# Kernel tuning notes

Measured on AMD Instinct MI355X. Metric: run time of the kernel, lower is better.

The kernel has to match this reference:

```python
import jax, jax.numpy as jnp
import numpy as np

B, N, D = 4, 4096, 512      # batch, seq_len, model width
DIM_K = 64                   # per-head key dim used ONLY for the 1/sqrt scale
PROJ = 512                   # dim_k*heads = dim_v*heads = 64*8


def setup_inputs() -> dict:
    key = jax.random.key(0)
    ks = jax.random.split(key, 11)
    glorot = lambda k, shape: jax.random.uniform(
        k, shape, jnp.float32,
        -np.sqrt(6.0 / (shape[0] + shape[1])), np.sqrt(6.0 / (shape[0] + shape[1])))
    return {
        "q": jax.random.normal(ks[0], (B, N, D), jnp.float32),
        "k": jax.random.normal(ks[1], (B, N, D), jnp.float32),
        "v": jax.random.normal(ks[2], (B, N, D), jnp.float32),
        "w_q": glorot(ks[3], (D, PROJ)),
        "w_k": glorot(ks[4], (D, PROJ)),
        "w_v": glorot(ks[5], (D, PROJ)),
        "w_mha": glorot(ks[6], (PROJ, D)),
        "b_q": jnp.zeros((1, 1, PROJ), jnp.float32),
        "b_k": jnp.zeros((1, 1, PROJ), jnp.float32),
        "b_v": jnp.zeros((1, 1, PROJ), jnp.float32),
        "b_mha": jnp.zeros((1, 1, D), jnp.float32),
    }


def reference(q, k, v, w_q, w_k, w_v, w_mha, b_q, b_k, b_v, b_mha):
    # Projections (tensordot over last axis + broadcast bias)
    qp = jnp.einsum('bnd,de->bne', q, w_q) + b_q
    kp = jnp.einsum('bnd,de->bne', k, w_k) + b_k
    vp = jnp.einsum('bnd,de->bne', v, w_v) + b_v
    # NOTE: original call() forgets to pass heads=self.heads, so heads=1:
    # a single attention over the full PROJ width, scaled by sqrt(DIM_K).
    atts = jnp.einsum('bqe,bke->bqk', qp, kp) / np.sqrt(DIM_K).astype(np.float32)
    atts = jax.nn.softmax(atts, axis=-1)      # [B, N, N]
    dpa = jnp.einsum('bqk,bke->bqe', atts, vp)
    return jnp.einsum('bne,ed->bnd', dpa, w_mha) + b_mha
```

## Files before the change

kernel.cpp:

```cpp
#include <hip/hip_runtime.h>
#include <hip/hip_bf16.h>


typedef __attribute__((ext_vector_type(8))) short bf16x8;
typedef __attribute__((ext_vector_type(4))) float f32x4;

#define NB 4
#define NN 4096
#define ND 512

__device__ __forceinline__ f32x4 mfma16(bf16x8 a, bf16x8 b, f32x4 c) {
    return __builtin_amdgcn_mfma_f32_16x16x32_bf16(a, b, c, 0, 0, 0);
}
__device__ __forceinline__ short f2bf(float f) {
    __hip_bfloat16 h = __float2bfloat16(f);
    return *reinterpret_cast<short*>(&h);
}

typedef __attribute__((address_space(1))) const unsigned int gls_gt;
typedef __attribute__((address_space(3))) unsigned int gls_lt;
__device__ __forceinline__ void gll16(const void* g, void* l) {
    __builtin_amdgcn_global_load_lds((gls_gt*)g, (gls_lt*)l, 16, 0, 0);
}

#define DPP_ROR_STEP(V, CTRL, OP)                                              \
    {                                                                          \
        int _t = __builtin_amdgcn_update_dpp(0, __float_as_int(V), (CTRL),     \
                                             0xf, 0xf, true);                  \
        (V) = OP((V), __int_as_float(_t));                                     \
    }
__device__ __forceinline__ float faddf(float a, float b) { return a + b; }
__device__ __forceinline__ float rmax16(float v) {
    DPP_ROR_STEP(v, 0x128, fmaxf)
    DPP_ROR_STEP(v, 0x124, fmaxf)
    DPP_ROR_STEP(v, 0x122, fmaxf)
    DPP_ROR_STEP(v, 0x121, fmaxf)
    return v;
}
__device__ __forceinline__ float rsum16(float v) {
    DPP_ROR_STEP(v, 0x128, faddf)
    DPP_ROR_STEP(v, 0x124, faddf)
    DPP_ROR_STEP(v, 0x122, faddf)
    DPP_ROR_STEP(v, 0x121, faddf)
    return v;
}

struct Ptrs4 {
    const float* in[4];
    short* out[4];
};

__global__ void transpose_w(Ptrs4 p) {
    __shared__ short tile[32][33];
    const float* in = p.in[blockIdx.z];
    short* out = p.out[blockIdx.z];
    int r0 = blockIdx.y * 32, c0 = blockIdx.x * 32;
    int tx = threadIdx.x, ty = threadIdx.y;
    for (int i = 0; i < 32; i += 8)
        tile[ty + i][tx] = f2bf(in[(r0 + ty + i) * 512 + c0 + tx]);
    __syncthreads();
    for (int i = 0; i < 32; i += 8)
        out[(c0 + ty + i) * 512 + r0 + tx] = tile[tx][ty + i];
}

struct ProjArgs {
    const float* in[3];
    const short* wt[3];
    const float* bias[3];
    short* out[3];
};

__global__ __launch_bounds__(256, 2) void proj_gemm3(ProjArgs pp) {
    __shared__ __align__(1024) char As[2][16384];
    __shared__ __align__(1024) char Bs[2][16384];
    int z = blockIdx.z;
    const float* A32 = pp.in[z];
    const short* Bt = pp.wt[z];
    const float* bias = pp.bias[z];
    short* C = pp.out[z];

    int tid = threadIdx.x;
    int lane = tid & 63, w = tid >> 6;
    int l15 = lane & 15, l4 = lane >> 4;
    int wr2 = (w & 1) * 64, wc2 = (w >> 1) * 64;
    int m0 = blockIdx.x * 128, n0 = blockIdx.y * 128;
    f32x4 acc[16] = {};

    int sr = lane >> 3;
    int sd = ((lane & 7) ^ sr) << 3;

#define P_STAGE_B(BUF, KT)                                                  \
    {                                                                       \
        _Pragma("unroll")                                                   \
        for (int i = 0; i < 4; i++) {                                       \
            int rbase = i * 32 + w * 8;                                     \
            gll16(&Bt[(size_t)(n0 + rbase + sr) * 512 + (KT) + sd],         \
                  Bs[BUF] + rbase * 128);                                   \
        }                                                                   \
    }

    float4 areg[8];
    int arow = w * 32 + (lane >> 4);
    int akc = lane & 15;
#define P_LOAD_A32(KT)                                                      \
    {                                                                       \
        _Pragma("unroll")                                                   \
        for (int inst = 0; inst < 8; inst++)                                \
            areg[inst] = ((const float4*)(A32 +                             \
                (size_t)(m0 + arow + inst * 4) * 512 + (KT)))[akc];         \
    }
#define P_WRITE_A32(BUF)                                                    \
    {                                                                       \
        _Pragma("unroll")                                                   \
        for (int inst = 0; inst < 8; inst++) {                              \
            int r = arow + inst * 4;                                        \
            short pk[4];                                                    \
            pk[0] = f2bf(areg[inst].x); pk[1] = f2bf(areg[inst].y);         \
            pk[2] = f2bf(areg[inst].z); pk[3] = f2bf(areg[inst].w);         \
            *(long long*)(As[BUF] + r * 128 +                               \
                (((akc >> 1) ^ (r & 7)) << 4) + ((akc & 1) << 3)) =         \
                *(const long long*)pk;                                      \
        }                                                                   \
    }

    P_LOAD_A32(0);
    P_STAGE_B(0, 0);
    P_WRITE_A32(0);
    for (int t = 0; t < 8; t++) {
        __syncthreads();
        if (t < 7) {
            P_LOAD_A32((t + 1) * 64);
            P_STAGE_B((t + 1) & 1, (t + 1) * 64);
        }
        const char* Ab = As[t & 1];
        const char* Bb = Bs[t & 1];
#pragma unroll
        for (int kb = 0; kb < 2; kb++) {
            int ph = ((((kb << 2) | l4) ^ (l15 & 7)) << 4);
            bf16x8 af[4], bfr[4];
#pragma unroll
            for (int mi = 0; mi < 4; mi++)
                af[mi] = *(const bf16x8*)(Ab + (wr2 + mi * 16 + l15) * 128 + ph);
#pragma unroll
            for (int ni = 0; ni < 4; ni++)
                bfr[ni] = *(const bf16x8*)(Bb + (wc2 + ni * 16 + l15) * 128 + ph);
#pragma unroll
            for (int mi = 0; mi < 4; mi++)
#pragma unroll
                for (int ni = 0; ni < 4; ni++)
                    acc[mi * 4 + ni] = mfma16(af[mi], bfr[ni], acc[mi * 4 + ni]);
        }
        if (t < 7) P_WRITE_A32((t + 1) & 1);
    }
#undef P_STAGE_B
#undef P_LOAD_A32
#undef P_WRITE_A32
    if (z == 2) {
        __syncthreads();
        short* Ct = (short*)As;
#pragma unroll
        for (int mi = 0; mi < 4; mi++)
#pragma unroll
            for (int ni = 0; ni < 4; ni++) {
                f32x4 vv = acc[mi * 4 + ni];
                int col = wc2 + ni * 16 + l15;
                float bv = bias[n0 + col];
                int r0w = wr2 + mi * 16 + l4 * 4;
                short pk[4];
#pragma unroll
                for (int r = 0; r < 4; r++) pk[r] = f2bf(vv[r] + bv);
                int byteoff = col * 256 + ((r0w * 2) ^ ((col & 7) << 4));
                *(long long*)((char*)Ct + byteoff) = *(const long long*)pk;
            }
        __syncthreads();
        int b = m0 >> 12;
        short* Cb = C + (size_t)b * (ND * NN) + (m0 & 4095);
#pragma unroll
        for (int s = 0; s < 8; s++) {
            int col = (tid >> 4) + 16 * s;
            int j = tid & 15;
            int byteoff = col * 256 + ((16 * j) ^ ((col & 7) << 4));
            bf16x8 vvv = *(const bf16x8*)((char*)Ct + byteoff);
            *(bf16x8*)(Cb + (size_t)(n0 + col) * NN + 8 * j) = vvv;
        }
    } else {
        __syncthreads();
        short* Ct = (short*)As;
#pragma unroll
        for (int mi = 0; mi < 4; mi++)
#pragma unroll
            for (int ni = 0; ni < 4; ni++) {
                f32x4 vv = acc[mi * 4 + ni];
                int col = wc2 + ni * 16 + l15;
                float bv = bias[n0 + col];
#pragma unroll
                for (int r = 0; r < 4; r++) {
                    int row = wr2 + mi * 16 + l4 * 4 + r;
                    int byteoff = row * 256 + ((col * 2) ^ ((row & 3) << 5));
                    *(short*)((char*)Ct + byteoff) = f2bf(vv[r] + bv);
                }
            }
        __syncthreads();
#pragma unroll
        for (int s = 0; s < 8; s++) {
            int row = (tid >> 4) + 16 * s;
            int j = tid & 15;
            int byteoff = row * 256 + ((16 * j) ^ ((row & 3) << 5));
            bf16x8 vvv = *(const bf16x8*)((char*)Ct + byteoff);
            *(bf16x8*)(C + (size_t)(m0 + row) * 512 + n0 + 8 * j) = vvv;
        }
    }
}

template <int AF32, int VT, int OF32>
__global__ __launch_bounds__(256, 2) void gemm_bt_bias(
    const void* __restrict__ Av, const short* __restrict__ Bt,
    const float* __restrict__ bias, void* __restrict__ C) {
    __shared__ __align__(1024) char As[2][16384];
    __shared__ __align__(1024) char Bs[2][16384];
    int tid = threadIdx.x;
    int lane = tid & 63, w = tid >> 6;
    int l15 = lane & 15, l4 = lane >> 4;
    int wr2 = (w & 1) * 64, wc2 = (w >> 1) * 64;
    int m0 = blockIdx.x * 128, n0 = blockIdx.y * 128;
    f32x4 acc[16] = {};

    int sr = lane >> 3;
    int sd = ((lane & 7) ^ sr) << 3;

#define STAGE_B(BUF, KT)                                                    \
    {                                                                       \
        _Pragma("unroll")                                                   \
        for (int i = 0; i < 4; i++) {                                       \
            int rbase = i * 32 + w * 8;                                     \
            gll16(&Bt[(size_t)(n0 + rbase + sr) * 512 + (KT) + sd],         \
                  Bs[BUF] + rbase * 128);                                   \
        }                                                                   \
    }
#define STAGE_A16(BUF, KT)                                                  \
    {                                                                       \
        const short* A16 = (const short*)Av;                                \
        _Pragma("unroll")                                                   \
        for (int i = 0; i < 4; i++) {                                       \
            int rbase = i * 32 + w * 8;                                     \
            gll16(&A16[(size_t)(m0 + rbase + sr) * 512 + (KT) + sd],        \
                  As[BUF] + rbase * 128);                                   \
        }                                                                   \
    }

    STAGE_A16(0, 0);
    STAGE_B(0, 0);
    for (int t = 0; t < 8; t++) {
        __syncthreads();
        if (t < 7) {
            STAGE_A16((t + 1) & 1, (t + 1) * 64);
            STAGE_B((t + 1) & 1, (t + 1) * 64);
        }
        const char* Ab = As[t & 1];
        const char* Bb = Bs[t & 1];
#pragma unroll
        for (int kb = 0; kb < 2; kb++) {
            int ph = ((((kb << 2) | l4) ^ (l15 & 7)) << 4);
            bf16x8 af[4], bfr[4];
#pragma unroll
            for (int mi = 0; mi < 4; mi++)
                af[mi] = *(const bf16x8*)(Ab + (wr2 + mi * 16 + l15) * 128 + ph);
#pragma unroll
            for (int ni = 0; ni < 4; ni++)
                bfr[ni] = *(const bf16x8*)(Bb + (wc2 + ni * 16 + l15) * 128 + ph);
#pragma unroll
            for (int mi = 0; mi < 4; mi++)
#pragma unroll
                for (int ni = 0; ni < 4; ni++)
                    acc[mi * 4 + ni] = mfma16(af[mi], bfr[ni], acc[mi * 4 + ni]);
        }
    }
#undef STAGE_B
#undef STAGE_A16
    for (int mi = 0; mi < 4; mi++)
        for (int ni = 0; ni < 4; ni++) {
            f32x4 vv = acc[mi * 4 + ni];
            int col = n0 + wc2 + ni * 16 + l15;
            float bv = bias[col];
            for (int r = 0; r < 4; r++) {
                int row = m0 + wr2 + mi * 16 + l4 * 4 + r;
                ((float*)C)[(size_t)row * 512 + col] = vv[r] + bv;
            }
        }
}

__global__ __launch_bounds__(512, 2) void flash_attn(
    const short* __restrict__ qp, const short* __restrict__ kp,
    const short* __restrict__ vpT, short* __restrict__ dpa) {
    __shared__ __align__(1024) char KsB[65536];
    __shared__ __align__(1024) char VsB[65536];
    __shared__ __align__(16)   char PldB[8192];
    __shared__ float SexM[128];
    __shared__ float SexS[128];

    int tid = threadIdx.x;
    int lane = tid & 63, w = tid >> 6;
    int l15 = lane & 15, l4 = lane >> 4;
    int wr = w & 3;
    int wc = w >> 2;
    int b = blockIdx.y;
    int q0 = blockIdx.x * 64;

    const short* qpb = qp + b * (NN * ND);
    const short* kpb = kp + b * (NN * ND);
    const short* vtb = vpT + b * (ND * NN);

    bf16x8 qf[16];
    {
        const short* qrow = qpb + (q0 + wr * 16 + l15) * ND + l4 * 8;
#pragma unroll
        for (int kb = 0; kb < 16; kb++) qf[kb] = *(const bf16x8*)(qrow + kb * 32);
    }
    f32x4 oacc[16] = {};
    float m_run[4], l_run[4];
#pragma unroll
    for (int r = 0; r < 4; r++) { m_run[r] = -1e30f; l_run[r] = 0.f; }

    const int vsl0 = ((l4 ^ (l15 & 7)) << 4);
    const int vsl1 = vsl0 ^ 64;

#define STAGE_K(J0)                                                         \
    {                                                                       \
        _Pragma("unroll")                                                   \
        for (int c = 0; c < 8; c++) {                                       \
            int key = w * 8 + c;                                            \
            const short* src = kpb + (size_t)((J0) + key) * ND +            \
                               ((lane ^ (key & 15)) << 3);                  \
            gll16(src, KsB + key * 1024);                                   \
        }                                                                   \
    }
#define STAGE_V(J0)                                                         \
    {                                                                       \
        _Pragma("unroll")                                                   \
        for (int c = 0; c < 8; c++) {                                       \
            int g = w * 8 + c;                                              \
            int e = g * 8 + (lane >> 3);                                    \
            const short* src = vtb + (size_t)e * NN + (J0) +                \
                               (((lane & 7) ^ (e & 7)) << 3);               \
            gll16(src, VsB + g * 1024);                                     \
        }                                                                   \
    }

    STAGE_K(0);
    STAGE_V(0);
    __syncthreads();

    for (int j0 = 0; j0 < NN; j0 += 64) {
        f32x4 s0 = {}, s1 = {};
        {
            const char* kb0 = KsB + (32 * wc + l15) * 1024;
            const char* kb1 = kb0 + 16 * 1024;
#pragma unroll
            for (int kb = 0; kb < 16; kb++) {
                int sl = ((((kb << 2) | l4) ^ l15) << 4);
                s0 = mfma16(qf[kb], *(const bf16x8*)(kb0 + sl), s0);
                s1 = mfma16(qf[kb], *(const bf16x8*)(kb1 + sl), s1);
            }
        }
        float vv0[4], vv1[4], mx[4], ss[4], p0[4], p1[4];
#pragma unroll
        for (int r = 0; r < 4; r++) {
            vv0[r] = s0[r] * 0.125f;
            vv1[r] = s1[r] * 0.125f;
            mx[r] = rmax16(fmaxf(vv0[r], vv1[r]));
        }
#pragma unroll
        for (int r = 0; r < 4; r++) {
            p0[r] = __expf(vv0[r] - mx[r]);
            p1[r] = __expf(vv1[r] - mx[r]);
            ss[r] = rsum16(p0[r] + p1[r]);
        }
        int row4 = wr * 16 + l4 * 4;
        if (l15 == 0) {
#pragma unroll
            for (int r = 0; r < 4; r++) {
                SexM[wc * 64 + row4 + r] = mx[r];
                SexS[wc * 64 + row4 + r] = ss[r];
            }
        }
        __syncthreads();
        float al4[4];
#pragma unroll
        for (int r = 0; r < 4; r++) {
            int row = row4 + r;
            float mo = SexM[(wc ^ 1) * 64 + row];
            float so = SexS[(wc ^ 1) * 64 + row];
            float mt = fmaxf(mx[r], mo);
            float st = ss[r] * __expf(mx[r] - mt) + so * __expf(mo - mt);
            float mn = fmaxf(m_run[r], mt);
            float al = __expf(m_run[r] - mn);
            l_run[r] = l_run[r] * al + st * __expf(mt - mn);
            m_run[r] = mn;
            al4[r] = al;
            float fs = __expf(mx[r] - mn);
            int rw7 = row & 7;
            char* prow = PldB + row * 128;
            int col0 = wc * 32 + l15;
            *(short*)(prow + (((col0 >> 3) ^ rw7) << 4) + ((col0 & 7) << 1)) = f2bf(p0[r] * fs);
            int col1 = col0 + 16;
            *(short*)(prow + (((col1 >> 3) ^ rw7) << 4) + ((col1 & 7) << 1)) = f2bf(p1[r] * fs);
        }
        {
            bool need = (al4[0] != 1.f) | (al4[1] != 1.f) |
                        (al4[2] != 1.f) | (al4[3] != 1.f);
            if (__any(need)) {
#pragma unroll
                for (int t = 0; t < 16; t++)
#pragma unroll
                    for (int r = 0; r < 4; r++) oacc[t][r] *= al4[r];
            }
        }
        __syncthreads();
        if (j0 + 64 < NN) STAGE_K(j0 + 64);
        bf16x8 pa0, pa1;
        {
            const char* prow = PldB + (wr * 16 + l15) * 128;
            pa0 = *(const bf16x8*)(prow + vsl0);
            pa1 = *(const bf16x8*)(prow + vsl1);
        }
#pragma unroll
        for (int eh = 0; eh < 2; eh++) {
#pragma unroll
            for (int i = 0; i < 8; i++) {
                const char* vb = VsB + (eh * 256 + 32 * i + 16 * wc + l15) * 128;
                int oi = eh * 8 + i;
                oacc[oi] = mfma16(pa0, *(const bf16x8*)(vb + vsl0), oacc[oi]);
                oacc[oi] = mfma16(pa1, *(const bf16x8*)(vb + vsl1), oacc[oi]);
            }
        }
        __syncthreads();
        if (j0 + 64 < NN) STAGE_V(j0 + 64);
    }
    float li[4];
#pragma unroll
    for (int r = 0; r < 4; r++) li[r] = 1.f / l_run[r];
    short* dpb = dpa + b * (NN * ND);
#pragma unroll
    for (int eh = 0; eh < 2; eh++)
#pragma unroll
        for (int i = 0; i < 8; i++) {
            int col = (16 * eh + 2 * i + wc) * 16 + l15;
#pragma unroll
            for (int r = 0; r < 4; r++) {
                int row = q0 + wr * 16 + l4 * 4 + r;
                dpb[row * ND + col] = f2bf(oacc[eh * 8 + i][r] * li[r]);
            }
        }
}

extern "C" void kernel_launch(void* const* d_in, const int* in_sizes, int n_in,
                              void* d_out, int out_size, void* d_ws, size_t ws_size,
                              hipStream_t stream) {
    const float* q     = (const float*)d_in[0];
    const float* k     = (const float*)d_in[1];
    const float* v     = (const float*)d_in[2];
    const float* w_q   = (const float*)d_in[3];
    const float* w_k   = (const float*)d_in[4];
    const float* w_v   = (const float*)d_in[5];
    const float* w_mha = (const float*)d_in[6];
    const float* b_q   = (const float*)d_in[7];
    const float* b_k   = (const float*)d_in[8];
    const float* b_v   = (const float*)d_in[9];
    const float* b_mha = (const float*)d_in[10];

    const size_t T = (size_t)NB * NN * ND;
    short* ws  = (short*)d_ws;
    short* qp  = ws;
    short* kp  = qp + T;
    short* vpT = kp + T;
    short* dpa = vpT + T;
    short* Wt  = dpa + T;

    Ptrs4 p;
    p.in[0] = w_q;   p.out[0] = Wt;
    p.in[1] = w_k;   p.out[1] = Wt + 262144;
    p.in[2] = w_v;   p.out[2] = Wt + 524288;
    p.in[3] = w_mha; p.out[3] = Wt + 786432;
    transpose_w<<<dim3(16, 16, 4), dim3(32, 8), 0, stream>>>(p);

    ProjArgs pa;
    pa.in[0] = q;  pa.wt[0] = Wt;          pa.bias[0] = b_q; pa.out[0] = qp;
    pa.in[1] = k;  pa.wt[1] = Wt + 262144; pa.bias[1] = b_k; pa.out[1] = kp;
    pa.in[2] = v;  pa.wt[2] = Wt + 524288; pa.bias[2] = b_v; pa.out[2] = vpT;
    proj_gemm3<<<dim3(128, 4, 3), 256, 0, stream>>>(pa);

    flash_attn<<<dim3(64, 4), 512, 0, stream>>>(qp, kp, vpT, dpa);

    gemm_bt_bias<0, 0, 1><<<dim3(128, 4), 256, 0, stream>>>(dpa, Wt + 786432, b_mha, d_out);
}
```

Baseline: 457.4 us.

## Shrink flash-attention tiles to 32 queries × 32 keys with 4 waves per block

Moves flash_attn from 64-query blocks of 8 waves with 64-key tiles to 32-query blocks of 4 waves with 32-key tiles, which doubles the grid to 512 blocks. LDS use drops to about 66KB per block, so more blocks can sit on each CU and the 256 CUs get better coverage. In exchange each K/V tile is reused by fewer queries, so K/V traffic from L2 doubles and there are twice as many loop iterations with barriers. The LDS swizzles and the P/V fragment indexing are reworked to fit the smaller tiles.

```diff
diff --git a/kernel.cpp b/kernel.cpp
--- a/kernel.cpp
+++ b/kernel.cpp
@@ -289,22 +289,22 @@
         }
 }
 
-__global__ __launch_bounds__(512, 2) void flash_attn(
+__global__ __launch_bounds__(256, 2) void flash_attn(
     const short* __restrict__ qp, const short* __restrict__ kp,
     const short* __restrict__ vpT, short* __restrict__ dpa) {
-    __shared__ __align__(1024) char KsB[65536];
-    __shared__ __align__(1024) char VsB[65536];
-    __shared__ __align__(16)   char PldB[8192];
-    __shared__ float SexM[128];
-    __shared__ float SexS[128];
+    __shared__ __align__(1024) char KsB[32768];
+    __shared__ __align__(1024) char VsB[32768];
+    __shared__ __align__(16)   char PldB[2048];
+    __shared__ float SexM[64];
+    __shared__ float SexS[64];
 
     int tid = threadIdx.x;
     int lane = tid & 63, w = tid >> 6;
     int l15 = lane & 15, l4 = lane >> 4;
-    int wr = w & 3;
-    int wc = w >> 2;
+    int wr = w & 1;
+    int wc = w >> 1;
     int b = blockIdx.y;
-    int q0 = blockIdx.x * 64;
+    int q0 = blockIdx.x * 32;
 
     const short* qpb = qp + b * (NN * ND);
     const short* kpb = kp + b * (NN * ND);
@@ -320,9 +320,6 @@
     float m_run[4], l_run[4];
 #pragma unroll
     for (int r = 0; r < 4; r++) { m_run[r] = -1e30f; l_run[r] = 0.f; }
-
-    const int vsl0 = ((l4 ^ (l15 & 7)) << 4);
-    const int vsl1 = vsl0 ^ 64;
 
 #define STAGE_K(J0)                                                         \
     {                                                                       \
@@ -339,9 +336,9 @@
         _Pragma("unroll")                                                   \
         for (int c = 0; c < 8; c++) {                                       \
             int g = w * 8 + c;                                              \
-            int e = g * 8 + (lane >> 3);                                    \
-            const short* src = vtb + (size_t)e * NN + (J0) +                \
-                               (((lane & 7) ^ (e & 7)) << 3);               \
+            int e = g * 16 + (lane >> 2);                                   \
+            int d = (lane & 3) ^ ((e >> 1) & 3);                            \
+            const short* src = vtb + (size_t)e * NN + (J0) + (d << 3);      \
             gll16(src, VsB + g * 1024);                                     \
         }                                                                   \
     }
@@ -350,37 +347,33 @@
     STAGE_V(0);
     __syncthreads();
 
-    for (int j0 = 0; j0 < NN; j0 += 64) {
-        f32x4 s0 = {}, s1 = {};
+    for (int j0 = 0; j0 < NN; j0 += 32) {
+        f32x4 s0 = {};
         {
-            const char* kb0 = KsB + (32 * wc + l15) * 1024;
-            const char* kb1 = kb0 + 16 * 1024;
+            const char* kb0 = KsB + (16 * wc + l15) * 1024;
 #pragma unroll
             for (int kb = 0; kb < 16; kb++) {
                 int sl = ((((kb << 2) | l4) ^ l15) << 4);
                 s0 = mfma16(qf[kb], *(const bf16x8*)(kb0 + sl), s0);
-                s1 = mfma16(qf[kb], *(const bf16x8*)(kb1 + sl), s1);
-            }
-        }
-        float vv0[4], vv1[4], mx[4], ss[4], p0[4], p1[4];
+            }
+        }
+        float vv[4], mx[4], ss[4], p0[4];
 #pragma unroll
         for (int r = 0; r < 4; r++) {
-            vv0[r] = s0[r] * 0.125f;
-            vv1[r] = s1[r] * 0.125f;
-            mx[r] = rmax16(fmaxf(vv0[r], vv1[r]));
+            vv[r] = s0[r] * 0.125f;
+            mx[r] = rmax16(vv[r]);
         }
 #pragma unroll
         for (int r = 0; r < 4; r++) {
-            p0[r] = __expf(vv0[r] - mx[r]);
-            p1[r] = __expf(vv1[r] - mx[r]);
-            ss[r] = rsum16(p0[r] + p1[r]);
+            p0[r] = __expf(vv[r] - mx[r]);
+            ss[r] = rsum16(p0[r]);
         }
         int row4 = wr * 16 + l4 * 4;
         if (l15 == 0) {
 #pragma unroll
             for (int r = 0; r < 4; r++) {
-                SexM[wc * 64 + row4 + r] = mx[r];
-                SexS[wc * 64 + row4 + r] = ss[r];
+                SexM[wc * 32 + row4 + r] = mx[r];
+                SexS[wc * 32 + row4 + r] = ss[r];
             }
         }
         __syncthreads();
@@ -388,8 +381,8 @@
 #pragma unroll
         for (int r = 0; r < 4; r++) {
             int row = row4 + r;
-            float mo = SexM[(wc ^ 1) * 64 + row];
-            float so = SexS[(wc ^ 1) * 64 + row];
+            float mo = SexM[(wc ^ 1) * 32 + row];
+            float so = SexS[(wc ^ 1) * 32 + row];
             float mt = fmaxf(mx[r], mo);
             float st = ss[r] * __expf(mx[r] - mt) + so * __expf(mo - mt);
             float mn = fmaxf(m_run[r], mt);
@@ -398,59 +391,50 @@
             m_run[r] = mn;
             al4[r] = al;
             float fs = __expf(mx[r] - mn);
-            int rw7 = row & 7;
-            char* prow = PldB + row * 128;
-            int col0 = wc * 32 + l15;
-            *(short*)(prow + (((col0 >> 3) ^ rw7) << 4) + ((col0 & 7) << 1)) = f2bf(p0[r] * fs);
-            int col1 = col0 + 16;
-            *(short*)(prow + (((col1 >> 3) ^ rw7) << 4) + ((col1 & 7) << 1)) = f2bf(p1[r] * fs);
+            int c0 = wc * 16 + l15;
+            *(short*)(PldB + row * 64 + (((c0 >> 3) ^ ((row >> 1) & 3)) << 4) +
+                      ((c0 & 7) << 1)) = f2bf(p0[r] * fs);
         }
         {
             bool need = (al4[0] != 1.f) | (al4[1] != 1.f) |
                         (al4[2] != 1.f) | (al4[3] != 1.f);
             if (__any(need)) {
 #pragma unroll
-                for (int t = 0; t < 16; t++)
-#pragma unroll
-                    for (int r = 0; r < 4; r++) oacc[t][r] *= al4[r];
-            }
-        }
-        __syncthreads();
-        if (j0 + 64 < NN) STAGE_K(j0 + 64);
-        bf16x8 pa0, pa1;
+                for (int i = 0; i < 16; i++)
+#pragma unroll
+                    for (int r = 0; r < 4; r++) oacc[i][r] *= al4[r];
+            }
+        }
+        __syncthreads();
+        if (j0 + 32 < NN) STAGE_K(j0 + 32);
         {
-            const char* prow = PldB + (wr * 16 + l15) * 128;
-            pa0 = *(const bf16x8*)(prow + vsl0);
-            pa1 = *(const bf16x8*)(prow + vsl1);
-        }
-#pragma unroll
-        for (int eh = 0; eh < 2; eh++) {
-#pragma unroll
-            for (int i = 0; i < 8; i++) {
-                const char* vb = VsB + (eh * 256 + 32 * i + 16 * wc + l15) * 128;
-                int oi = eh * 8 + i;
-                oacc[oi] = mfma16(pa0, *(const bf16x8*)(vb + vsl0), oacc[oi]);
-                oacc[oi] = mfma16(pa1, *(const bf16x8*)(vb + vsl1), oacc[oi]);
-            }
-        }
-        __syncthreads();
-        if (j0 + 64 < NN) STAGE_V(j0 + 64);
+            int prow = wr * 16 + l15;
+            bf16x8 pa = *(const bf16x8*)(
+                PldB + prow * 64 + ((l4 ^ ((prow >> 1) & 3)) << 4));
+#pragma unroll
+            for (int i = 0; i < 16; i++) {
+                int e = (2 * i + wc) * 16 + l15;
+                const bf16x8* vb = (const bf16x8*)(
+                    VsB + e * 64 + ((l4 ^ ((e >> 1) & 3)) << 4));
+                oacc[i] = mfma16(pa, *vb, oacc[i]);
+            }
+        }
+        __syncthreads();
+        if (j0 + 32 < NN) STAGE_V(j0 + 32);
     }
     float li[4];
 #pragma unroll
     for (int r = 0; r < 4; r++) li[r] = 1.f / l_run[r];
     short* dpb = dpa + b * (NN * ND);
 #pragma unroll
-    for (int eh = 0; eh < 2; eh++)
-#pragma unroll
-        for (int i = 0; i < 8; i++) {
-            int col = (16 * eh + 2 * i + wc) * 16 + l15;
-#pragma unroll
-            for (int r = 0; r < 4; r++) {
-                int row = q0 + wr * 16 + l4 * 4 + r;
-                dpb[row * ND + col] = f2bf(oacc[eh * 8 + i][r] * li[r]);
-            }
-        }
+    for (int i = 0; i < 16; i++) {
+        int col = (2 * i + wc) * 16 + l15;
+#pragma unroll
+        for (int r = 0; r < 4; r++) {
+            int row = q0 + wr * 16 + l4 * 4 + r;
+            dpb[row * ND + col] = f2bf(oacc[i][r] * li[r]);
+        }
+    }
 }
 
 extern "C" void kernel_launch(void* const* d_in, const int* in_sizes, int n_in,
@@ -489,7 +473,7 @@
     pa.in[2] = v;  pa.wt[2] = Wt + 524288; pa.bias[2] = b_v; pa.out[2] = vpT;
     proj_gemm3<<<dim3(128, 4, 3), 256, 0, stream>>>(pa);
 
-    flash_attn<<<dim3(64, 4), 512, 0, stream>>>(qp, kp, vpT, dpa);
+    flash_attn<<<dim3(128, 4), 256, 0, stream>>>(qp, kp, vpT, dpa);
 
     gemm_bt_bias<0, 0, 1><<<dim3(128, 4), 256, 0, stream>>>(dpa, Wt + 786432, b_mha, d_out);
 }
```

After: 531.1 us. 16.1% more time.
